# Kernel optimization log

Hardware: AMD Instinct MI355X
Metric: run time of the kernel (lower is better)

The kernel has to match this reference:

```python
import jax, jax.numpy as jnp
import numpy as np

S, M, E = 8192, 2048, 64          # tokens, model_dim, num_experts
CAP = 2 * S // E                   # GShard top-2 capacity = 2S/E = 256


def setup_inputs() -> dict:
    key = jax.random.key(0)
    k1, k2, k3 = jax.random.split(key, 3)
    x = jax.random.normal(k1, (S, M), dtype=jnp.float32)
    # torch.nn.Linear weight layout: [out_features, in_features] = [E, M]
    wg = jax.random.normal(k2, (E, M), dtype=jnp.float32) * np.float32(1.0 / np.sqrt(M))
    u = jax.random.uniform(k3, (S, E), dtype=jnp.float32, minval=1e-6, maxval=1.0 - 1e-6)
    gumbel = -jnp.log(-jnp.log(u))  # standard Gumbel(0,1) noise for 2nd-expert sampling
    return {"x": x, "wg": wg, "gumbel": gumbel}


def top2gating(logits, gumbel):
    # logits: [S, E]
    gates = jax.nn.softmax(logits.astype(jnp.float32), axis=1)

    # top-1 expert
    idx1 = jnp.argmax(gates, axis=1)                        # [S]
    mask1 = jax.nn.one_hot(idx1, E, dtype=jnp.int32)        # [S, E]

    # top-2 expert: argmax over gumbel-noised logits with top-1 masked out
    logits_except1 = jnp.where(mask1.astype(bool), -jnp.inf, logits + gumbel)
    idx2 = jnp.argmax(logits_except1, axis=1)
    mask2 = jax.nn.one_hot(idx2, E, dtype=jnp.int32)

    # positions within each expert's buffer (capacity cumsum)
    loc1 = jnp.cumsum(mask1, axis=0) - 1                    # [S, E]
    loc2 = jnp.cumsum(mask2, axis=0) - 1 + jnp.sum(mask1, axis=0, keepdims=True)

    # load-balancing auxiliary loss
    me = jnp.mean(gates, axis=0)                            # [E]
    ce = jnp.mean(mask1.astype(jnp.float32), axis=0)        # [E]
    l_aux = jnp.mean(me * ce) * np.float32(E * E)

    # drop tokens that exceed capacity
    mask1 = mask1 * (loc1 < CAP).astype(jnp.int32)
    mask2 = mask2 * (loc2 < CAP).astype(jnp.int32)

    loc1_s = jnp.sum(loc1 * mask1, axis=1)                  # [S]
    loc2_s = jnp.sum(loc2 * mask2, axis=1)

    m1f = mask1.astype(jnp.float32)
    m2f = mask2.astype(jnp.float32)

    # normalized top-2 gate values
    g1 = jnp.sum(gates * m1f, axis=1)                       # [S]
    g2 = jnp.sum(gates * m2f, axis=1)
    denom = jnp.maximum(g1 + g2, jnp.finfo(jnp.float32).eps)
    g1 = g1 / denom
    g2 = g2 / denom

    gates1 = g1[:, None] * m1f                              # [S, E]
    gates2 = g2[:, None] * m2f

    loc1_sc = jax.nn.one_hot(loc1_s, CAP, dtype=jnp.float32)  # [S, C]
    loc2_sc = jax.nn.one_hot(loc2_s, CAP, dtype=jnp.float32)

    combine_weights = (jnp.einsum('se,sc->sec', gates1, loc1_sc)
                       + jnp.einsum('se,sc->sec', gates2, loc2_sc))  # [S, E, C]
    dispatch_mask = combine_weights > 0
    return l_aux, combine_weights, dispatch_mask


def reference(x, wg, gumbel):
    logits = x @ wg.T                                       # [S, E]
    return top2gating(logits, gumbel)
```

## Files before the change

kernel.cpp:

```cpp
#include <hip/hip_runtime.h>
#include <cstdint>
#include <cstddef>

#define S_TOK 8192
#define MDIM  2048
#define NEXP  64
#define CAPTY 256
#define NCHUNK 128

#define GEMM_BLOCKS 256
#define FILL_BLOCKS 2048

__global__ __launch_bounds__(256) void fill_and_gemm(
    const float* __restrict__ x, const float* __restrict__ wg,
    float* __restrict__ outA, float* __restrict__ outB,
    float* __restrict__ out) {
  const int bid = blockIdx.x;
  const int t = threadIdx.x;

  if (bid >= GEMM_BLOCKS) {
    const int fb = bid - GEMM_BLOCKS;
    float4 z = {0.f, 0.f, 0.f, 0.f};
    float4* o4 = reinterpret_cast<float4*>(out);
    size_t idx = (size_t)fb * 256 + t;
#pragma unroll 8
    for (int i = 0; i < 128; ++i) {
      o4[idx] = z;
      idx += (size_t)FILL_BLOCKS * 256;
    }
    if (fb == 0 && t == 0) out[268435456] = 0.f;
    return;
  }

  __shared__ float xs[64][36];
  __shared__ float wsh[64][36];
  const int half = bid & 1;
  const int rowBase = (bid >> 1) * 64;
  const int kHalf = half * 1024;
  const int tx = t & 15;
  const int ty = t >> 4;
  float acc[4][4] = {{0.f}};

  const int rStage = t >> 3;
  const int cStage = (t & 7) << 2;

  for (int kt = 0; kt < 1024; kt += 32) {
    const int kBase = kHalf + kt;
    for (int rr = rStage; rr < 64; rr += 32) {
      float4 xv = *reinterpret_cast<const float4*>(
          &x[(size_t)(rowBase + rr) * MDIM + kBase + cStage]);
      *reinterpret_cast<float4*>(&xs[rr][cStage]) = xv;
      float4 wv = *reinterpret_cast<const float4*>(
          &wg[(size_t)rr * MDIM + kBase + cStage]);
      *reinterpret_cast<float4*>(&wsh[rr][cStage]) = wv;
    }
    __syncthreads();
#pragma unroll
    for (int k = 0; k < 32; k += 4) {
      float4 xa[4], wb[4];
#pragma unroll
      for (int a = 0; a < 4; ++a)
        xa[a] = *reinterpret_cast<const float4*>(&xs[ty * 4 + a][k]);
#pragma unroll
      for (int b = 0; b < 4; ++b)
        wb[b] = *reinterpret_cast<const float4*>(&wsh[tx + 16 * b][k]);
#pragma unroll
      for (int a = 0; a < 4; ++a)
#pragma unroll
        for (int b = 0; b < 4; ++b) {
          acc[a][b] += xa[a].x * wb[b].x;
          acc[a][b] += xa[a].y * wb[b].y;
          acc[a][b] += xa[a].z * wb[b].z;
          acc[a][b] += xa[a].w * wb[b].w;
        }
    }
    __syncthreads();
  }
  float* o = half ? outB : outA;
#pragma unroll
  for (int a = 0; a < 4; ++a)
#pragma unroll
    for (int b = 0; b < 4; ++b)
      o[(size_t)(rowBase + ty * 4 + a) * NEXP + tx + 16 * b] = acc[a][b];
}

__global__ __launch_bounds__(1024) void gate_rank(
    const float* __restrict__ la, const float* __restrict__ lb,
    const float* __restrict__ gum,
    int* __restrict__ e1o, int* __restrict__ e2o,
    float* __restrict__ g1o, float* __restrict__ g2o,
    float* __restrict__ me_part,
    int* __restrict__ w1, int* __restrict__ w2,
    int* __restrict__ hist1, int* __restrict__ hist2) {
  __shared__ float me_l[NEXP];
  __shared__ int e1_l[64], e2_l[64];
  const int c = blockIdx.x;
  const int t = threadIdx.x;
  const int w = t >> 6;
  const int lane = t & 63;
  if (t < NEXP) me_l[t] = 0.f;
  __syncthreads();

  float me_acc = 0.f;
#pragma unroll
  for (int i = 0; i < 4; ++i) {
    const int s = c * 64 + w * 4 + i;
    const size_t base = (size_t)s * NEXP + lane;
    const float l = la[base] + lb[base];
    const float gn = gum[base];

    float m = l;
#pragma unroll
    for (int d = 1; d < 64; d <<= 1) m = fmaxf(m, __shfl_xor(m, d, 64));
    const float p = expf(l - m);
    float sum = p;
#pragma unroll
    for (int d = 1; d < 64; d <<= 1) sum += __shfl_xor(sum, d, 64);

    unsigned long long b1 = __ballot(l == m);
    const int e1 = __ffsll(b1) - 1;

    const float y = (lane == e1) ? -INFINITY : (l + gn);
    float m2 = y;
#pragma unroll
    for (int d = 1; d < 64; d <<= 1) m2 = fmaxf(m2, __shfl_xor(m2, d, 64));
    unsigned long long b2 = __ballot(y == m2);
    const int e2 = __ffsll(b2) - 1;

    const float p1 = __shfl(p, e1, 64);
    const float p2 = __shfl(p, e2, 64);

    me_acc += p / sum;

    if (lane == 0) {
      e1o[s] = e1;
      e2o[s] = e2;
      g1o[s] = p1;
      g2o[s] = p2;
      e1_l[w * 4 + i] = e1;
      e2_l[w * 4 + i] = e2;
    }
  }
  atomicAdd(&me_l[lane], me_acc);
  __syncthreads();

  if (w == 0) {
    const int a = e1_l[lane];
    const int b = e2_l[lane];
    const unsigned long long lt = (1ull << lane) - 1ull;
    int r1 = 0, r2 = 0;
    for (int e = 0; e < NEXP; ++e) {
      unsigned long long m1 = __ballot(a == e);
      unsigned long long m2 = __ballot(b == e);
      if (a == e) r1 = __popcll(m1 & lt);
      if (b == e) r2 = __popcll(m2 & lt);
      if (lane == e) {
        hist1[c * NEXP + e] = __popcll(m1);
        hist2[c * NEXP + e] = __popcll(m2);
      }
    }
    w1[c * 64 + lane] = r1;
    w2[c * 64 + lane] = r2;
  }
  if (t < NEXP) me_part[c * NEXP + t] = me_l[t];
}

__global__ __launch_bounds__(64) void prefix_aux(
    const int* __restrict__ hist1, const int* __restrict__ hist2,
    const float* __restrict__ me_part,
    int* __restrict__ off1, int* __restrict__ off2,
    float* __restrict__ out0) {
  const int e = threadIdx.x;
  int run = 0;
  for (int c = 0; c < NCHUNK; ++c) {
    off1[c * NEXP + e] = run;
    run += hist1[c * NEXP + e];
  }
  const int tot1 = run;
  int run2 = tot1;
  for (int c = 0; c < NCHUNK; ++c) {
    off2[c * NEXP + e] = run2;
    run2 += hist2[c * NEXP + e];
  }
  float ms = 0.f;
  for (int c = 0; c < NCHUNK; ++c) ms += me_part[c * NEXP + e];
  float la = ms * (float)tot1;
#pragma unroll
  for (int d = 1; d < 64; d <<= 1) la += __shfl_xor(la, d, 64);
  if (e == 0)
    out0[0] = la * (float)NEXP / ((float)S_TOK * (float)S_TOK);
}

__global__ __launch_bounds__(256) void scatter(
    const int* __restrict__ e1, const int* __restrict__ e2,
    const int* __restrict__ w1, const int* __restrict__ w2,
    const float* __restrict__ g1r, const float* __restrict__ g2r,
    const int* __restrict__ off1, const int* __restrict__ off2,
    float* __restrict__ out) {
  const int s = blockIdx.x * 256 + threadIdx.x;
  const int c = s >> 6;
  const int a = e1[s];
  const int b = e2[s];
  const int l1 = off1[c * NEXP + a] + w1[s];
  const int l2 = off2[c * NEXP + b] + w2[s];
  const bool k1 = l1 < CAPTY;
  const bool k2 = l2 < CAPTY;
  float p1 = k1 ? g1r[s] : 0.f;
  float p2 = k2 ? g2r[s] : 0.f;
  const float denom = p1 + p2;
  if (denom > 0.f) {
    const float inv = 1.f / denom;
    float* cw = out + 1;
    float* dm = out + 1 + (size_t)S_TOK * NEXP * CAPTY;
    const size_t rowb = (size_t)s * NEXP * CAPTY;
    if (k1) {
      const size_t i1 = rowb + (size_t)a * CAPTY + l1;
      cw[i1] = p1 * inv;
      dm[i1] = 1.f;
    }
    if (k2) {
      const size_t i2 = rowb + (size_t)b * CAPTY + l2;
      cw[i2] = p2 * inv;
      dm[i2] = 1.f;
    }
  }
}

extern "C" void kernel_launch(void* const* d_in, const int* in_sizes, int n_in,
                              void* d_out, int out_size, void* d_ws,
                              size_t ws_size, hipStream_t stream) {
  const float* x = (const float*)d_in[0];
  const float* wg = (const float*)d_in[1];
  const float* gum = (const float*)d_in[2];
  float* out = (float*)d_out;

  char* w = (char*)d_ws;
  size_t off = 0;
  float* logitsA = (float*)(w + off); off += (size_t)S_TOK * NEXP * 4;
  float* logitsB = (float*)(w + off); off += (size_t)S_TOK * NEXP * 4;
  int*   e1   = (int*)(w + off); off += (size_t)S_TOK * 4;
  int*   e2   = (int*)(w + off); off += (size_t)S_TOK * 4;
  float* g1r  = (float*)(w + off); off += (size_t)S_TOK * 4;
  float* g2r  = (float*)(w + off); off += (size_t)S_TOK * 4;
  int*   w1   = (int*)(w + off); off += (size_t)S_TOK * 4;
  int*   w2   = (int*)(w + off); off += (size_t)S_TOK * 4;
  int*   hist1 = (int*)(w + off); off += (size_t)NCHUNK * NEXP * 4;
  int*   hist2 = (int*)(w + off); off += (size_t)NCHUNK * NEXP * 4;
  int*   off1 = (int*)(w + off); off += (size_t)NCHUNK * NEXP * 4;
  int*   off2 = (int*)(w + off); off += (size_t)NCHUNK * NEXP * 4;
  float* me_part = (float*)(w + off); off += (size_t)NCHUNK * NEXP * 4;

  fill_and_gemm<<<GEMM_BLOCKS + FILL_BLOCKS, 256, 0, stream>>>(
      x, wg, logitsA, logitsB, out);
  gate_rank<<<NCHUNK, 1024, 0, stream>>>(logitsA, logitsB, gum, e1, e2, g1r,
                                         g2r, me_part, w1, w2, hist1, hist2);
  prefix_aux<<<1, 64, 0, stream>>>(hist1, hist2, me_part, off1, off2, out);
  scatter<<<S_TOK / 256, 256, 0, stream>>>(e1, e2, w1, w2, g1r, g2r, off1,
                                           off2, out);
}
```

Before: 1.149 ms.

## Fuse gating into the GEMM kernel and parallelize the prefix scan with wave shuffles

Folds the per-chunk softmax, top-2 selection and ranking into the GEMM blocks, so logits stay in shared memory rather than passing through global buffers, and one kernel launch is removed. The GEMM now runs as 128 blocks that each do the full K range, where before it was 256 blocks split over two K halves. The histogram, offset and me_part arrays are transposed to an expert-major layout. This lets prefix_aux replace its serial 128-step loops with wave-wide shuffle scans. The cost is half as many GEMM blocks, with longer per-block serial work alongside the zero-fill blocks.

```diff
diff --git a/kernel.cpp b/kernel.cpp
--- a/kernel.cpp
+++ b/kernel.cpp
@@ -8,18 +8,22 @@
 #define CAPTY 256
 #define NCHUNK 128
 
-#define GEMM_BLOCKS 256
+#define CHUNK_BLOCKS 128
 #define FILL_BLOCKS 2048
 
-__global__ __launch_bounds__(256) void fill_and_gemm(
+__global__ __launch_bounds__(256) void moe_mega(
     const float* __restrict__ x, const float* __restrict__ wg,
-    float* __restrict__ outA, float* __restrict__ outB,
-    float* __restrict__ out) {
+    const float* __restrict__ gum, float* __restrict__ out,
+    int* __restrict__ e1o, int* __restrict__ e2o,
+    float* __restrict__ g1o, float* __restrict__ g2o,
+    int* __restrict__ w1, int* __restrict__ w2,
+    int* __restrict__ hist1T, int* __restrict__ hist2T,
+    float* __restrict__ me_partT) {
   const int bid = blockIdx.x;
   const int t = threadIdx.x;
 
-  if (bid >= GEMM_BLOCKS) {
-    const int fb = bid - GEMM_BLOCKS;
+  if (bid >= CHUNK_BLOCKS) {
+    const int fb = bid - CHUNK_BLOCKS;
     float4 z = {0.f, 0.f, 0.f, 0.f};
     float4* o4 = reinterpret_cast<float4*>(out);
     size_t idx = (size_t)fb * 256 + t;
@@ -34,25 +38,28 @@
 
   __shared__ float xs[64][36];
   __shared__ float wsh[64][36];
-  const int half = bid & 1;
-  const int rowBase = (bid >> 1) * 64;
-  const int kHalf = half * 1024;
+  __shared__ float lg[64][65];
+  __shared__ float me_l[NEXP];
+  __shared__ int e1_l[64], e2_l[64];
+  __shared__ float g1_l[64], g2_l[64];
+
+  const int c = bid;
+  const int rowBase = c * 64;
   const int tx = t & 15;
   const int ty = t >> 4;
-  float acc[4][4] = {{0.f}};
-
   const int rStage = t >> 3;
   const int cStage = (t & 7) << 2;
 
+  float acc[4][4] = {{0.f}};
+
   for (int kt = 0; kt < 1024; kt += 32) {
-    const int kBase = kHalf + kt;
     for (int rr = rStage; rr < 64; rr += 32) {
-      float4 xv = *reinterpret_cast<const float4*>(
-          &x[(size_t)(rowBase + rr) * MDIM + kBase + cStage]);
-      *reinterpret_cast<float4*>(&xs[rr][cStage]) = xv;
-      float4 wv = *reinterpret_cast<const float4*>(
-          &wg[(size_t)rr * MDIM + kBase + cStage]);
-      *reinterpret_cast<float4*>(&wsh[rr][cStage]) = wv;
+      *reinterpret_cast<float4*>(&xs[rr][cStage]) =
+          *reinterpret_cast<const float4*>(
+              &x[(size_t)(rowBase + rr) * MDIM + kt + cStage]);
+      *reinterpret_cast<float4*>(&wsh[rr][cStage]) =
+          *reinterpret_cast<const float4*>(
+              &wg[(size_t)rr * MDIM + kt + cStage]);
     }
     __syncthreads();
 #pragma unroll
@@ -76,38 +83,63 @@
     }
     __syncthreads();
   }
-  float* o = half ? outB : outA;
 #pragma unroll
   for (int a = 0; a < 4; ++a)
 #pragma unroll
+    for (int b = 0; b < 4; ++b) {
+      lg[ty * 4 + a][tx + 16 * b] = acc[a][b];
+      acc[a][b] = 0.f;
+    }
+
+  for (int kt = 1024; kt < 2048; kt += 32) {
+    for (int rr = rStage; rr < 64; rr += 32) {
+      *reinterpret_cast<float4*>(&xs[rr][cStage]) =
+          *reinterpret_cast<const float4*>(
+              &x[(size_t)(rowBase + rr) * MDIM + kt + cStage]);
+      *reinterpret_cast<float4*>(&wsh[rr][cStage]) =
+          *reinterpret_cast<const float4*>(
+              &wg[(size_t)rr * MDIM + kt + cStage]);
+    }
+    __syncthreads();
+#pragma unroll
+    for (int k = 0; k < 32; k += 4) {
+      float4 xa[4], wb[4];
+#pragma unroll
+      for (int a = 0; a < 4; ++a)
+        xa[a] = *reinterpret_cast<const float4*>(&xs[ty * 4 + a][k]);
+#pragma unroll
+      for (int b = 0; b < 4; ++b)
+        wb[b] = *reinterpret_cast<const float4*>(&wsh[tx + 16 * b][k]);
+#pragma unroll
+      for (int a = 0; a < 4; ++a)
+#pragma unroll
+        for (int b = 0; b < 4; ++b) {
+          acc[a][b] += xa[a].x * wb[b].x;
+          acc[a][b] += xa[a].y * wb[b].y;
+          acc[a][b] += xa[a].z * wb[b].z;
+          acc[a][b] += xa[a].w * wb[b].w;
+        }
+    }
+    __syncthreads();
+  }
+#pragma unroll
+  for (int a = 0; a < 4; ++a)
+#pragma unroll
     for (int b = 0; b < 4; ++b)
-      o[(size_t)(rowBase + ty * 4 + a) * NEXP + tx + 16 * b] = acc[a][b];
-}
-
-__global__ __launch_bounds__(1024) void gate_rank(
-    const float* __restrict__ la, const float* __restrict__ lb,
-    const float* __restrict__ gum,
-    int* __restrict__ e1o, int* __restrict__ e2o,
-    float* __restrict__ g1o, float* __restrict__ g2o,
-    float* __restrict__ me_part,
-    int* __restrict__ w1, int* __restrict__ w2,
-    int* __restrict__ hist1, int* __restrict__ hist2) {
-  __shared__ float me_l[NEXP];
-  __shared__ int e1_l[64], e2_l[64];
-  const int c = blockIdx.x;
-  const int t = threadIdx.x;
-  const int w = t >> 6;
-  const int lane = t & 63;
+      lg[ty * 4 + a][tx + 16 * b] += acc[a][b];
+
   if (t < NEXP) me_l[t] = 0.f;
   __syncthreads();
 
+  const int wv = t >> 6;
+  const int lane = t & 63;
   float me_acc = 0.f;
-#pragma unroll
-  for (int i = 0; i < 4; ++i) {
-    const int s = c * 64 + w * 4 + i;
-    const size_t base = (size_t)s * NEXP + lane;
-    const float l = la[base] + lb[base];
-    const float gn = gum[base];
+#pragma unroll 1
+  for (int i = 0; i < 16; ++i) {
+    const int tok = wv * 16 + i;
+    const int s = rowBase + tok;
+    const float l = lg[tok][lane];
+    const float gn = gum[(size_t)s * NEXP + lane];
 
     float m = l;
 #pragma unroll
@@ -133,18 +165,24 @@
     me_acc += p / sum;
 
     if (lane == 0) {
-      e1o[s] = e1;
-      e2o[s] = e2;
-      g1o[s] = p1;
-      g2o[s] = p2;
-      e1_l[w * 4 + i] = e1;
-      e2_l[w * 4 + i] = e2;
+      e1_l[tok] = e1;
+      e2_l[tok] = e2;
+      g1_l[tok] = p1;
+      g2_l[tok] = p2;
     }
   }
   atomicAdd(&me_l[lane], me_acc);
   __syncthreads();
 
-  if (w == 0) {
+  if (t < 64) {
+    e1o[rowBase + t] = e1_l[t];
+    e2o[rowBase + t] = e2_l[t];
+    g1o[rowBase + t] = g1_l[t];
+    g2o[rowBase + t] = g2_l[t];
+    me_partT[(size_t)t * NCHUNK + c] = me_l[t];
+  }
+
+  if (wv == 0) {
     const int a = e1_l[lane];
     const int b = e2_l[lane];
     const unsigned long long lt = (1ull << lane) - 1ull;
@@ -155,54 +193,82 @@
       if (a == e) r1 = __popcll(m1 & lt);
       if (b == e) r2 = __popcll(m2 & lt);
       if (lane == e) {
-        hist1[c * NEXP + e] = __popcll(m1);
-        hist2[c * NEXP + e] = __popcll(m2);
+        hist1T[e * NCHUNK + c] = __popcll(m1);
+        hist2T[e * NCHUNK + c] = __popcll(m2);
       }
     }
-    w1[c * 64 + lane] = r1;
-    w2[c * 64 + lane] = r2;
-  }
-  if (t < NEXP) me_part[c * NEXP + t] = me_l[t];
+    w1[rowBase + lane] = r1;
+    w2[rowBase + lane] = r2;
+  }
 }
 
 __global__ __launch_bounds__(64) void prefix_aux(
-    const int* __restrict__ hist1, const int* __restrict__ hist2,
-    const float* __restrict__ me_part,
-    int* __restrict__ off1, int* __restrict__ off2,
+    const int* __restrict__ hist1T, const int* __restrict__ hist2T,
+    const float* __restrict__ me_partT,
+    int* __restrict__ off1T, int* __restrict__ off2T,
     float* __restrict__ out0) {
-  const int e = threadIdx.x;
-  int run = 0;
-  for (int c = 0; c < NCHUNK; ++c) {
-    off1[c * NEXP + e] = run;
-    run += hist1[c * NEXP + e];
-  }
-  const int tot1 = run;
-  int run2 = tot1;
-  for (int c = 0; c < NCHUNK; ++c) {
-    off2[c * NEXP + e] = run2;
-    run2 += hist2[c * NEXP + e];
-  }
-  float ms = 0.f;
-  for (int c = 0; c < NCHUNK; ++c) ms += me_part[c * NEXP + e];
-  float la = ms * (float)tot1;
-#pragma unroll
-  for (int d = 1; d < 64; d <<= 1) la += __shfl_xor(la, d, 64);
-  if (e == 0)
-    out0[0] = la * (float)NEXP / ((float)S_TOK * (float)S_TOK);
+  const int lane = threadIdx.x;
+  float la_acc = 0.f;
+  for (int e = 0; e < NEXP; ++e) {
+    const int h0 = hist1T[e * NCHUNK + lane];
+    const int h1 = hist1T[e * NCHUNK + 64 + lane];
+    int s0 = h0;
+#pragma unroll
+    for (int d = 1; d < 64; d <<= 1) {
+      int v = __shfl_up(s0, d, 64);
+      if (lane >= d) s0 += v;
+    }
+    const int tot0 = __shfl(s0, 63, 64);
+    int s1 = h1;
+#pragma unroll
+    for (int d = 1; d < 64; d <<= 1) {
+      int v = __shfl_up(s1, d, 64);
+      if (lane >= d) s1 += v;
+    }
+    s1 += tot0;
+    const int tot1 = __shfl(s1, 63, 64);
+    off1T[e * NCHUNK + lane] = s0 - h0;
+    off1T[e * NCHUNK + 64 + lane] = s1 - h1;
+
+    const int h2a = hist2T[e * NCHUNK + lane];
+    const int h2b = hist2T[e * NCHUNK + 64 + lane];
+    int s2a = h2a;
+#pragma unroll
+    for (int d = 1; d < 64; d <<= 1) {
+      int v = __shfl_up(s2a, d, 64);
+      if (lane >= d) s2a += v;
+    }
+    const int tot2a = __shfl(s2a, 63, 64);
+    int s2b = h2b;
+#pragma unroll
+    for (int d = 1; d < 64; d <<= 1) {
+      int v = __shfl_up(s2b, d, 64);
+      if (lane >= d) s2b += v;
+    }
+    off2T[e * NCHUNK + lane] = tot1 + s2a - h2a;
+    off2T[e * NCHUNK + 64 + lane] = tot1 + tot2a + s2b - h2b;
+
+    float ms = me_partT[e * NCHUNK + lane] + me_partT[e * NCHUNK + 64 + lane];
+#pragma unroll
+    for (int d = 1; d < 64; d <<= 1) ms += __shfl_xor(ms, d, 64);
+    if (lane == 0) la_acc += ms * (float)tot1;
+  }
+  if (lane == 0)
+    out0[0] = la_acc * (float)NEXP / ((float)S_TOK * (float)S_TOK);
 }
 
 __global__ __launch_bounds__(256) void scatter(
     const int* __restrict__ e1, const int* __restrict__ e2,
     const int* __restrict__ w1, const int* __restrict__ w2,
     const float* __restrict__ g1r, const float* __restrict__ g2r,
-    const int* __restrict__ off1, const int* __restrict__ off2,
+    const int* __restrict__ off1T, const int* __restrict__ off2T,
     float* __restrict__ out) {
   const int s = blockIdx.x * 256 + threadIdx.x;
   const int c = s >> 6;
   const int a = e1[s];
   const int b = e2[s];
-  const int l1 = off1[c * NEXP + a] + w1[s];
-  const int l2 = off2[c * NEXP + b] + w2[s];
+  const int l1 = off1T[a * NCHUNK + c] + w1[s];
+  const int l2 = off2T[b * NCHUNK + c] + w2[s];
   const bool k1 = l1 < CAPTY;
   const bool k2 = l2 < CAPTY;
   float p1 = k1 ? g1r[s] : 0.f;
@@ -236,25 +302,22 @@
 
   char* w = (char*)d_ws;
   size_t off = 0;
-  float* logitsA = (float*)(w + off); off += (size_t)S_TOK * NEXP * 4;
-  float* logitsB = (float*)(w + off); off += (size_t)S_TOK * NEXP * 4;
   int*   e1   = (int*)(w + off); off += (size_t)S_TOK * 4;
   int*   e2   = (int*)(w + off); off += (size_t)S_TOK * 4;
   float* g1r  = (float*)(w + off); off += (size_t)S_TOK * 4;
   float* g2r  = (float*)(w + off); off += (size_t)S_TOK * 4;
   int*   w1   = (int*)(w + off); off += (size_t)S_TOK * 4;
   int*   w2   = (int*)(w + off); off += (size_t)S_TOK * 4;
-  int*   hist1 = (int*)(w + off); off += (size_t)NCHUNK * NEXP * 4;
-  int*   hist2 = (int*)(w + off); off += (size_t)NCHUNK * NEXP * 4;
-  int*   off1 = (int*)(w + off); off += (size_t)NCHUNK * NEXP * 4;
-  int*   off2 = (int*)(w + off); off += (size_t)NCHUNK * NEXP * 4;
-  float* me_part = (float*)(w + off); off += (size_t)NCHUNK * NEXP * 4;
-
-  fill_and_gemm<<<GEMM_BLOCKS + FILL_BLOCKS, 256, 0, stream>>>(
-      x, wg, logitsA, logitsB, out);
-  gate_rank<<<NCHUNK, 1024, 0, stream>>>(logitsA, logitsB, gum, e1, e2, g1r,
-                                         g2r, me_part, w1, w2, hist1, hist2);
-  prefix_aux<<<1, 64, 0, stream>>>(hist1, hist2, me_part, off1, off2, out);
-  scatter<<<S_TOK / 256, 256, 0, stream>>>(e1, e2, w1, w2, g1r, g2r, off1,
-                                           off2, out);
+  int*   hist1T = (int*)(w + off); off += (size_t)NEXP * NCHUNK * 4;
+  int*   hist2T = (int*)(w + off); off += (size_t)NEXP * NCHUNK * 4;
+  int*   off1T  = (int*)(w + off); off += (size_t)NEXP * NCHUNK * 4;
+  int*   off2T  = (int*)(w + off); off += (size_t)NEXP * NCHUNK * 4;
+  float* me_partT = (float*)(w + off); off += (size_t)NEXP * NCHUNK * 4;
+
+  moe_mega<<<CHUNK_BLOCKS + FILL_BLOCKS, 256, 0, stream>>>(
+      x, wg, gum, out, e1, e2, g1r, g2r, w1, w2, hist1T, hist2T, me_partT);
+  prefix_aux<<<1, 64, 0, stream>>>(hist1T, hist2T, me_partT, off1T, off2T,
+                                   out);
+  scatter<<<S_TOK / 256, 256, 0, stream>>>(e1, e2, w1, w2, g1r, g2r, off1T,
+                                           off2T, out);
 }
```

Result: slower. 1.277 ms (+11.1%).
